# Optimization experiments

Hardware: AMD Instinct MI355X
Metric: run time of the kernel (lower is better)

Reference implementation:

```python
import jax, jax.numpy as jnp
import numpy as np

NV, NC, E, H, L = 100_000, 420_000, 630_000, 128, 8
ALPHA, THETA = 0.1, 0.5


def _seg_mean(msgs, dst, n_dst):
    # mean aggregation over destination segments (PyG SAGEConv default)
    s = jax.ops.segment_sum(msgs, dst, num_segments=n_dst)
    cnt = jax.ops.segment_sum(jnp.ones((dst.shape[0], 1), msgs.dtype), dst, num_segments=n_dst)
    return s / jnp.maximum(cnt, 1.0)


def _sage(x_src, x_dst, src, dst, n_dst, Wl, bl, Wr):
    # SAGEConv: lin_l(mean_{j in N(i)} x_j) + lin_r(x_i); lin_r has no bias
    agg = _seg_mean(x_src[src], dst, n_dst)
    return agg @ Wl + bl + x_dst @ Wr


def setup_inputs() -> dict:
    key = jax.random.key(0)
    ks = jax.random.split(key, 40)
    k = iter(range(40))
    rn = lambda shape, s=0.05: jax.random.normal(ks[next(k)], shape, jnp.float32) * s
    inp = {}
    inp['x_variable'] = jax.random.normal(ks[next(k)], (NV, 4), jnp.float32)
    inp['x_clause'] = jax.random.normal(ks[next(k)], (NC, 1), jnp.float32)
    src_p = jax.random.randint(ks[next(k)], (E,), 0, NV)
    dst_p = jax.random.randint(ks[next(k)], (E,), 0, NC)
    src_n = jax.random.randint(ks[next(k)], (E,), 0, NV)
    dst_n = jax.random.randint(ks[next(k)], (E,), 0, NC)
    inp['edge_pos'] = jnp.stack([src_p, dst_p])  # variable -> clause
    inp['edge_neg'] = jnp.stack([src_n, dst_n])
    inp['W_vemb'] = rn((4, H)); inp['b_vemb'] = rn((H,))
    inp['W_cemb'] = rn((1, H)); inp['b_cemb'] = rn((H,))
    for tag in ('pos', 'neg', 'rpos', 'rneg'):
        inp[f'Wl_{tag}'] = rn((L, H, H)); inp[f'bl_{tag}'] = rn((L, H))
        inp[f'Wr_{tag}'] = rn((L, H, H))
    inp['Wv'] = rn((L, H, H)); inp['bv'] = rn((L, H))
    inp['W_fin'] = rn((H, 1)); inp['b_fin'] = rn((1,))
    return inp


def reference(x_variable, x_clause, edge_pos, edge_neg,
              W_vemb, b_vemb, W_cemb, b_cemb,
              Wl_pos, bl_pos, Wr_pos, Wl_neg, bl_neg, Wr_neg,
              Wl_rpos, bl_rpos, Wr_rpos, Wl_rneg, bl_rneg, Wr_rneg,
              Wv, bv, W_fin, b_fin):
    v_h0 = jax.nn.relu(x_variable @ W_vemb + b_vemb)
    c_h0 = jax.nn.relu(x_clause @ W_cemb + b_cemb)
    v_h, c_h = v_h0, c_h0
    sp, dp = edge_pos[0], edge_pos[1]
    sn, dn = edge_neg[0], edge_neg[1]
    for i in range(L):
        v_old = v_h
        # HeteroConv(aggr='sum'): clause gets pos_in + neg_in, variable gets rev_pos_in + rev_neg_in
        c_new = (_sage(v_h, c_h, sp, dp, NC, Wl_pos[i], bl_pos[i], Wr_pos[i]) +
                 _sage(v_h, c_h, sn, dn, NC, Wl_neg[i], bl_neg[i], Wr_neg[i]))
        v_new = (_sage(c_h, v_h, dp, sp, NV, Wl_rpos[i], bl_rpos[i], Wr_rpos[i]) +
                 _sage(c_h, v_h, dn, sn, NV, Wl_rneg[i], bl_rneg[i], Wr_rneg[i]))
        v_h = (1.0 - ALPHA) * v_new + ALPHA * v_h0
        c_h = (1.0 - ALPHA) * c_new + ALPHA * c_h0
        beta = float(np.log(THETA / (i + 1) + 1.0))
        v_h = (1.0 - beta) * v_h + beta * (v_h @ Wv[i] + bv[i])
        v_h = v_h + v_old  # use_inter_layer_res=True
        v_h, c_h = jax.nn.relu(v_h), jax.nn.relu(c_h)
    return v_h @ W_fin + b_fin
```

## Files before the change

### kernel.cpp

```cpp
#include <hip/hip_runtime.h>
#include <math.h>

#define NVV 100000
#define NCC 420000
#define EE  630000
#define HH  128
#define LL  8

typedef unsigned int uint;
typedef unsigned short ushort;
typedef __attribute__((ext_vector_type(8))) short bf16x8;
typedef __attribute__((ext_vector_type(4))) float f32x4;

#define MFMA16(a,b,c) __builtin_amdgcn_mfma_f32_16x16x32_bf16(a,b,c,0,0,0)
#define SW(r,k) (((r)<<7) + ((k) ^ (((r)&7)<<3)))

__device__ inline float bf2f(uint u){ return __uint_as_float(u << 16); }
__device__ inline uint  f2bf(float f){
  uint b = __float_as_uint(f);
  return (b + 0x7FFFu + ((b >> 16) & 1u)) >> 16;
}
__device__ inline uint pack2(float a, float b){ return f2bf(a) | (f2bf(b) << 16); }
__device__ inline float4 relu4(float4 v){
  v.x = fmaxf(v.x, 0.f); v.y = fmaxf(v.y, 0.f);
  v.z = fmaxf(v.z, 0.f); v.w = fmaxf(v.w, 0.f);
  return v;
}

__global__ void k_sentinel(float* out, float v){
  if (blockIdx.x == 0 && threadIdx.x == 0) out[0] = v;
}

__device__ inline float4 vemb4(const float* __restrict__ xv, const float* __restrict__ W,
                               const float* __restrict__ b, int i, int h4){
  float x0 = xv[4*i+0], x1 = xv[4*i+1], x2 = xv[4*i+2], x3 = xv[4*i+3];
  float4 w0 = *(const float4*)(W + 0*HH + h4);
  float4 w1 = *(const float4*)(W + 1*HH + h4);
  float4 w2 = *(const float4*)(W + 2*HH + h4);
  float4 w3 = *(const float4*)(W + 3*HH + h4);
  float4 bb = *(const float4*)(b + h4);
  float4 r;
  r.x = fmaf(x0,w0.x, fmaf(x1,w1.x, fmaf(x2,w2.x, fmaf(x3,w3.x, bb.x))));
  r.y = fmaf(x0,w0.y, fmaf(x1,w1.y, fmaf(x2,w2.y, fmaf(x3,w3.y, bb.y))));
  r.z = fmaf(x0,w0.z, fmaf(x1,w1.z, fmaf(x2,w2.z, fmaf(x3,w3.z, bb.z))));
  r.w = fmaf(x0,w0.w, fmaf(x1,w1.w, fmaf(x2,w2.w, fmaf(x3,w3.w, bb.w))));
  return r;
}

__global__ void k_embed_v(const float* __restrict__ xv, const float* __restrict__ W,
                          const float* __restrict__ b, float* __restrict__ out){
  int tid = blockIdx.x * 256 + threadIdx.x;
  int i = tid >> 5;
  if (i >= NVV) return;
  int h4 = (tid & 31) << 2;
  *(float4*)(out + (size_t)i*HH + h4) = relu4(vemb4(xv, W, b, i, h4));
}

__global__ void k_embed_c(const float* __restrict__ xc, const float* __restrict__ W,
                          const float* __restrict__ b, uint* __restrict__ out){
  int tid = blockIdx.x * 256 + threadIdx.x;
  int i = tid >> 5;
  if (i >= NCC) return;
  int c2 = tid & 31;
  int h4 = c2 << 2;
  float x0 = xc[i];
  float4 w = *(const float4*)(W + h4);
  float4 bb = *(const float4*)(b + h4);
  float4 r;
  r.x = fmaxf(fmaf(x0, w.x, bb.x), 0.f);
  r.y = fmaxf(fmaf(x0, w.y, bb.y), 0.f);
  r.z = fmaxf(fmaf(x0, w.z, bb.z), 0.f);
  r.w = fmaxf(fmaf(x0, w.w, bb.w), 0.f);
  uint2 o; o.x = pack2(r.x, r.y); o.y = pack2(r.z, r.w);
  *(uint2*)(out + (size_t)i*64 + c2*2) = o;
}

__global__ void k_prep(const float* __restrict__ Wl_pos, const float* __restrict__ Wl_neg,
                       const float* __restrict__ Wl_rpos, const float* __restrict__ Wl_rneg,
                       const float* __restrict__ Wv, const float* __restrict__ Wr_pos,
                       const float* __restrict__ Wr_neg, const float* __restrict__ Wr_rpos,
                       const float* __restrict__ Wr_rneg, ushort* __restrict__ wt){
  int tid = blockIdx.x * 256 + threadIdx.x;
  int n4 = tid & 31, k = (tid >> 5) & 127, l = (tid >> 12) & 7, m = tid >> 15;
  const float* s1; const float* s2 = nullptr;
  switch (m){
    case 0: s1 = Wl_pos;  break;
    case 1: s1 = Wl_neg;  break;
    case 2: s1 = Wl_rpos; break;
    case 3: s1 = Wl_rneg; break;
    case 4: s1 = Wv;      break;
    case 5: s1 = Wr_pos;  s2 = Wr_neg;  break;
    default: s1 = Wr_rpos; s2 = Wr_rneg; break;
  }
  size_t o = (size_t)l*16384 + (size_t)k*128 + n4*4;
  float4 w = *(const float4*)(s1 + o);
  if (s2){
    float4 w2 = *(const float4*)(s2 + o);
    w.x += w2.x; w.y += w2.y; w.z += w2.z; w.w += w2.w;
  }
  ushort* hi = wt + (size_t)((m*LL + l)*2    )*16384;
  ushort* lo = wt + (size_t)((m*LL + l)*2 + 1)*16384;
  float vv[4] = {w.x, w.y, w.z, w.w};
  #pragma unroll
  for (int e = 0; e < 4; ++e){
    int n = n4*4 + e;
    uint h = f2bf(vv[e]);
    float r = vv[e] - bf2f(h);
    hi[SW(n, k)] = (ushort)h;
    lo[SW(n, k)] = (ushort)f2bf(r);
  }
}

__global__ void k_counti(const int* __restrict__ d, int* cnt, int n){
  int i = blockIdx.x * 256 + threadIdx.x;
  if (i < n) atomicAdd(&cnt[d[i]], 1);
}

#define SCAN256(ts, t) \
  for (int off = 1; off < 256; off <<= 1){ \
    int _a = (t >= off) ? ts[t - off] : 0; \
    __syncthreads(); \
    ts[t] += _a; \
    __syncthreads(); \
  }

__global__ void k_scanb(const int* __restrict__ in, int* __restrict__ out,
                        int* __restrict__ part, int n){
  __shared__ int ts[256];
  int b = blockIdx.x, t = threadIdx.x;
  int base = b*1024 + t*4;
  int v0 = (base+0 < n) ? in[base+0] : 0;
  int v1 = (base+1 < n) ? in[base+1] : 0;
  int v2 = (base+2 < n) ? in[base+2] : 0;
  int v3 = (base+3 < n) ? in[base+3] : 0;
  int s1 = v0, s2 = s1+v1, s3 = s2+v2, tsum = s3+v3;
  ts[t] = tsum; __syncthreads();
  SCAN256(ts, t)
  int excl = ts[t] - tsum;
  if (base+0 < n) out[base+0] = excl;
  if (base+1 < n) out[base+1] = excl + s1;
  if (base+2 < n) out[base+2] = excl + s2;
  if (base+3 < n) out[base+3] = excl + s3;
  if (t == 255) part[b] = ts[255];
}

__global__ void k_scanp(int* p, int nb){
  __shared__ int ts[256];
  __shared__ int carry;
  int t = threadIdx.x;
  if (t == 0) carry = 0;
  __syncthreads();
  for (int c = 0; c*256 < nb; ++c){
    int i = c*256 + t;
    int v = (i < nb) ? p[i] : 0;
    ts[t] = v; __syncthreads();
    SCAN256(ts, t)
    int excl = ts[t] - v + carry;
    if (i < nb) p[i] = excl;
    int tot = ts[255];
    __syncthreads();
    if (t == 0) carry += tot;
    __syncthreads();
  }
}

__global__ void k_scana(int* out, const int* __restrict__ part, int n){
  int i = blockIdx.x * 256 + threadIdx.x;
  if (i < n) out[i] += part[i >> 10];
}

__global__ void k_fill(const int* __restrict__ dst, const int* __restrict__ pay,
                       int* cur, int* __restrict__ eo, int n){
  int i = blockIdx.x * 256 + threadIdx.x;
  if (i >= n) return;
  int p = atomicAdd(&cur[dst[i]], 1);
  eo[p] = pay[i];
}

__global__ void k_vgather(const uint* __restrict__ ch,
                          const int* __restrict__ ipp, const int* __restrict__ epp,
                          const int* __restrict__ ipn, const int* __restrict__ epn,
                          uint* __restrict__ Up, uint* __restrict__ Un){
  int g = blockIdx.x * 256 + threadIdx.x;
  int v = g >> 6, lane = g & 63;
  if (v >= NVV) return;
  int s = v ? ipp[v-1] : 0, e = ipp[v];
  float a0 = 0.f, a1 = 0.f;
  for (int j = s; j < e; ++j){
    uint u = ch[(size_t)epp[j]*64 + lane];
    a0 += bf2f(u & 0xFFFFu); a1 += bf2f(u >> 16);
  }
  float inv = 1.f / fmaxf((float)(e - s), 1.f);
  Up[(size_t)v*64 + lane] = pack2(a0*inv, a1*inv);
  s = v ? ipn[v-1] : 0; e = ipn[v];
  a0 = 0.f; a1 = 0.f;
  for (int j = s; j < e; ++j){
    uint u = ch[(size_t)epn[j]*64 + lane];
    a0 += bf2f(u & 0xFFFFu); a1 += bf2f(u >> 16);
  }
  inv = 1.f / fmaxf((float)(e - s), 1.f);
  Un[(size_t)v*64 + lane] = pack2(a0*inv, a1*inv);
}

__device__ inline void stA_bf16(const uint4* __restrict__ A, ushort* As, int m0, int M, int t){
  #pragma unroll
  for (int j = 0; j < 4; ++j){
    int idx = j*512 + t, r = idx >> 4, c = idx & 15;
    uint4 v = make_uint4(0,0,0,0);
    if (m0 + r < M) v = A[(size_t)(m0 + r)*16 + c];
    *(uint4*)(As + SW(r, c*8)) = v;
  }
}

__device__ inline void stA_f32(const float* __restrict__ A, ushort* As, int m0, int M, int t){
  const float4* A4 = (const float4*)A;
  #pragma unroll
  for (int j = 0; j < 8; ++j){
    int idx = j*512 + t, r = idx >> 5, c = idx & 31;
    float4 v = make_float4(0.f,0.f,0.f,0.f);
    if (m0 + r < M) v = A4[(size_t)(m0 + r)*32 + c];
    uint2 u; u.x = pack2(v.x, v.y); u.y = pack2(v.z, v.w);
    *(uint2*)(As + SW(r, c*4)) = u;
  }
}

__device__ inline void stB(const uint4* __restrict__ Bt, ushort* Bs, int t){
  #pragma unroll
  for (int j = 0; j < 4; ++j) ((uint4*)Bs)[j*512 + t] = Bt[j*512 + t];
}

__device__ inline void kloop(const ushort* As, const ushort* Bs, int wr, int wc,
                             int l15, int g, f32x4 acc[2][4]){
  #pragma unroll
  for (int kk = 0; kk < 4; ++kk){
    int kb = kk*32 + g*8;
    bf16x8 a0 = *(const bf16x8*)(As + SW(wr*32 + l15,      kb));
    bf16x8 a1 = *(const bf16x8*)(As + SW(wr*32 + 16 + l15, kb));
    #pragma unroll
    for (int ni = 0; ni < 4; ++ni){
      int n = wc*64 + ni*16 + l15;
      bf16x8 b = *(const bf16x8*)(Bs + SW(n, kb));
      acc[0][ni] = MFMA16(a0, b, acc[0][ni]);
      acc[1][ni] = MFMA16(a1, b, acc[1][ni]);
    }
  }
}

__device__ inline void accStoreF(float* ldsF, f32x4 acc[2][4], int wr, int wc, int l15, int g){
  #pragma unroll
  for (int mi = 0; mi < 2; ++mi)
    #pragma unroll
    for (int ni = 0; ni < 4; ++ni)
      #pragma unroll
      for (int j = 0; j < 4; ++j)
        ldsF[(wr*32 + mi*16 + g*4 + j)*128 + wc*64 + ni*16 + l15] = acc[mi][ni][j];
}

__device__ inline void accStoreFsw(float* ldsF, f32x4 acc[2][4], int wr, int wc, int l15, int g){
  #pragma unroll
  for (int mi = 0; mi < 2; ++mi)
    #pragma unroll
    for (int ni = 0; ni < 4; ++ni)
      #pragma unroll
      for (int j = 0; j < 4; ++j){
        int r = wr*32 + mi*16 + g*4 + j;
        int c = wc*64 + ni*16 + l15;
        ldsF[r*128 + (((c >> 2) ^ (r & 31)) << 2) + (c & 3)] = acc[mi][ni][j];
      }
}

__device__ inline void accStoreBf(ushort* dst, f32x4 acc[2][4], int wr, int wc, int l15, int g){
  #pragma unroll
  for (int mi = 0; mi < 2; ++mi)
    #pragma unroll
    for (int ni = 0; ni < 4; ++ni)
      #pragma unroll
      for (int j = 0; j < 4; ++j)
        dst[(wr*32 + mi*16 + g*4 + j)*128 + wc*64 + ni*16 + l15] =
            (ushort)f2bf(acc[mi][ni][j]);
}

#define MMHEAD \
  __shared__ ushort lds[32768]; \
  ushort* As = lds; ushort* Bs = lds + 16384; \
  int t = threadIdx.x, m0 = blockIdx.x * 128; \
  int w = t >> 6, l = t & 63, wr = w >> 1, wc = w & 1, l15 = l & 15, g = l >> 4; \
  const f32x4 zz = {0.f, 0.f, 0.f, 0.f};

__global__ __launch_bounds__(512) void k_mm_dual(const float* __restrict__ A,
    const uint4* __restrict__ Bph, const uint4* __restrict__ Bpl,
    const uint4* __restrict__ Bnh, const uint4* __restrict__ Bnl,
    uint4* __restrict__ Up, uint4* __restrict__ Un, int M){
  MMHEAD
  f32x4 accP[2][4], accN[2][4];
  #pragma unroll
  for (int mi = 0; mi < 2; ++mi)
    #pragma unroll
    for (int ni = 0; ni < 4; ++ni){ accP[mi][ni] = zz; accN[mi][ni] = zz; }
  stA_f32(A, As, m0, M, t);
  stB(Bph, Bs, t); __syncthreads();
  kloop(As, Bs, wr, wc, l15, g, accP); __syncthreads();
  stB(Bpl, Bs, t); __syncthreads();
  kloop(As, Bs, wr, wc, l15, g, accP); __syncthreads();
  stB(Bnh, Bs, t); __syncthreads();
  kloop(As, Bs, wr, wc, l15, g, accN); __syncthreads();
  stB(Bnl, Bs, t); __syncthreads();
  kloop(As, Bs, wr, wc, l15, g, accN); __syncthreads();
  accStoreBf(lds,         accP, wr, wc, l15, g);
  accStoreBf(lds + 16384, accN, wr, wc, l15, g);
  __syncthreads();
  #pragma unroll
  for (int j = 0; j < 4; ++j){
    int idx = j*512 + t, r = idx >> 4, c = idx & 15;
    if (m0 + r < M){
      Up[(size_t)(m0 + r)*16 + c] = ((const uint4*)lds)[idx];
      Un[(size_t)(m0 + r)*16 + c] = ((const uint4*)(lds + 16384))[idx];
    }
  }
}

__global__ __launch_bounds__(512) void k_mm3(const uint4* __restrict__ Ap,
    const uint4* __restrict__ An, const float* __restrict__ Af,
    const uint4* __restrict__ Bph, const uint4* __restrict__ Bpl,
    const uint4* __restrict__ Bnh, const uint4* __restrict__ Bnl,
    const uint4* __restrict__ Bfh, const uint4* __restrict__ Bfl,
    const float* __restrict__ xv, const float* __restrict__ Wve, const float* __restrict__ bve,
    const float* __restrict__ blp, const float* __restrict__ bln,
    uint2* __restrict__ vmid, int M){
  MMHEAD
  f32x4 acc[2][4];
  #pragma unroll
  for (int mi = 0; mi < 2; ++mi)
    #pragma unroll
    for (int ni = 0; ni < 4; ++ni) acc[mi][ni] = zz;

  stA_bf16(Ap, As, m0, M, t); stB(Bph, Bs, t); __syncthreads();
  kloop(As, Bs, wr, wc, l15, g, acc); __syncthreads();
  stB(Bpl, Bs, t); __syncthreads();
  kloop(As, Bs, wr, wc, l15, g, acc); __syncthreads();

  stA_bf16(An, As, m0, M, t); stB(Bnh, Bs, t); __syncthreads();
  kloop(As, Bs, wr, wc, l15, g, acc); __syncthreads();
  stB(Bnl, Bs, t); __syncthreads();
  kloop(As, Bs, wr, wc, l15, g, acc); __syncthreads();

  stA_f32(Af, As, m0, M, t); stB(Bfh, Bs, t); __syncthreads();
  kloop(As, Bs, wr, wc, l15, g, acc); __syncthreads();
  stB(Bfl, Bs, t); __syncthreads();
  kloop(As, Bs, wr, wc, l15, g, acc); __syncthreads();

  float* ldsF = (float*)lds;
  accStoreF(ldsF, acc, wr, wc, l15, g);
  __syncthreads();
  #pragma unroll
  for (int j = 0; j < 8; ++j){
    int idx = j*512 + t, r = idx >> 5, c4 = idx & 31;
    int row = m0 + r;
    if (row >= M) continue;
    float4 a4 = ((const float4*)ldsF)[r*32 + c4];
    float4 bp = ((const float4*)blp)[c4];
    float4 bn = ((const float4*)bln)[c4];
    float4 w0 = ((const float4*)Wve)[0*32 + c4];
    float4 w1 = ((const float4*)Wve)[1*32 + c4];
    float4 w2 = ((const float4*)Wve)[2*32 + c4];
    float4 w3 = ((const float4*)Wve)[3*32 + c4];
    float4 bb = ((const float4*)bve)[c4];
    float4 xx = *(const float4*)(xv + (size_t)row*4);
    float4 h;
    h.x = fmaf(xx.x,w0.x, fmaf(xx.y,w1.x, fmaf(xx.z,w2.x, fmaf(xx.w,w3.x, bb.x))));
    h.y = fmaf(xx.x,w0.y, fmaf(xx.y,w1.y, fmaf(xx.z,w2.y, fmaf(xx.w,w3.y, bb.y))));
    h.z = fmaf(xx.x,w0.z, fmaf(xx.y,w1.z, fmaf(xx.z,w2.z, fmaf(xx.w,w3.z, bb.z))));
    h.w = fmaf(xx.x,w0.w, fmaf(xx.y,w1.w, fmaf(xx.z,w2.w, fmaf(xx.w,w3.w, bb.w))));
    h = relu4(h);
    float4 o;
    o.x = 0.9f*(a4.x + bp.x + bn.x) + 0.1f*h.x;
    o.y = 0.9f*(a4.y + bp.y + bn.y) + 0.1f*h.y;
    o.z = 0.9f*(a4.z + bp.z + bn.z) + 0.1f*h.z;
    o.w = 0.9f*(a4.w + bp.w + bn.w) + 0.1f*h.w;
    uint2 u; u.x = pack2(o.x, o.y); u.y = pack2(o.z, o.w);
    vmid[(size_t)row*32 + c4] = u;
  }
}

__global__ __launch_bounds__(512) void k_mm_f(const uint4* __restrict__ Avm,
    const uint4* __restrict__ Bh, const uint4* __restrict__ Bl,
    const uint2* __restrict__ vmid, const float* __restrict__ bvv,
    float omb, float beta, float* vh, int M){
  MMHEAD
  f32x4 acc[2][4];
  #pragma unroll
  for (int mi = 0; mi < 2; ++mi)
    #pragma unroll
    for (int ni = 0; ni < 4; ++ni) acc[mi][ni] = zz;
  stA_bf16(Avm, As, m0, M, t); stB(Bh, Bs, t); __syncthreads();
  kloop(As, Bs, wr, wc, l15, g, acc); __syncthreads();
  stB(Bl, Bs, t); __syncthreads();
  kloop(As, Bs, wr, wc, l15, g, acc); __syncthreads();
  float* ldsF = (float*)lds;
  accStoreF(ldsF, acc, wr, wc, l15, g);
  __syncthreads();
  #pragma unroll
  for (int j = 0; j < 8; ++j){
    int idx = j*512 + t, r = idx >> 5, c4 = idx & 31;
    int row = m0 + r;
    if (row >= M) continue;
    float4 a4 = ((const float4*)ldsF)[r*32 + c4];
    uint2 um = vmid[(size_t)row*32 + c4];
    float4 bb = ((const float4*)bvv)[c4];
    float4 vo = *(const float4*)(vh + (size_t)row*HH + c4*4);
    float m0f = bf2f(um.x & 0xFFFFu), m1f = bf2f(um.x >> 16);
    float m2f = bf2f(um.y & 0xFFFFu), m3f = bf2f(um.y >> 16);
    float4 o;
    o.x = fmaxf(omb*m0f + beta*(a4.x + bb.x) + vo.x, 0.f);
    o.y = fmaxf(omb*m1f + beta*(a4.y + bb.y) + vo.y, 0.f);
    o.z = fmaxf(omb*m2f + beta*(a4.z + bb.z) + vo.z, 0.f);
    o.w = fmaxf(omb*m3f + beta*(a4.w + bb.w) + vo.w, 0.f);
    *(float4*)(vh + (size_t)row*HH + c4*4) = o;
  }
}

__global__ __launch_bounds__(512) void k_mm_c(const uint4* ch,
    const uint4* __restrict__ Bh, const uint4* __restrict__ Bl,
    const int* __restrict__ ipp, const int* __restrict__ epp,
    const int* __restrict__ ipn, const int* __restrict__ epn,
    const uint4* __restrict__ Yp, const uint4* __restrict__ Yn,
    const float* __restrict__ xc, const float* __restrict__ Wc, const float* __restrict__ bc,
    const float* __restrict__ blp, const float* __restrict__ bln,
    uint2* chout){
  MMHEAD
  f32x4 acc[2][4];
  #pragma unroll
  for (int mi = 0; mi < 2; ++mi)
    #pragma unroll
    for (int ni = 0; ni < 4; ++ni) acc[mi][ni] = zz;
  stA_bf16(ch, As, m0, NCC, t); stB(Bh, Bs, t); __syncthreads();
  kloop(As, Bs, wr, wc, l15, g, acc); __syncthreads();
  stB(Bl, Bs, t); __syncthreads();
  kloop(As, Bs, wr, wc, l15, g, acc); __syncthreads();
  float* ldsF = (float*)lds;
  accStoreFsw(ldsF, acc, wr, wc, l15, g);
  __syncthreads();

  int r = t >> 2, q = t & 3, row = m0 + r;
  if (row >= NCC) return;
  float4 ga[8];
  #pragma unroll
  for (int m = 0; m < 8; ++m) ga[m] = make_float4(0.f,0.f,0.f,0.f);
  int s = row ? ipp[row-1] : 0, e = ipp[row];
  for (int j = s; j < e; ++j){
    const uint4* yr = Yp + (size_t)epp[j]*16 + q*4;
    #pragma unroll
    for (int m = 0; m < 4; ++m){
      uint4 u = yr[m];
      ga[2*m].x   += bf2f(u.x & 0xFFFFu); ga[2*m].y   += bf2f(u.x >> 16);
      ga[2*m].z   += bf2f(u.y & 0xFFFFu); ga[2*m].w   += bf2f(u.y >> 16);
      ga[2*m+1].x += bf2f(u.z & 0xFFFFu); ga[2*m+1].y += bf2f(u.z >> 16);
      ga[2*m+1].z += bf2f(u.w & 0xFFFFu); ga[2*m+1].w += bf2f(u.w >> 16);
    }
  }
  float invp = 1.f / fmaxf((float)(e - s), 1.f);
  #pragma unroll
  for (int m = 0; m < 8; ++m){
    ga[m].x *= invp; ga[m].y *= invp; ga[m].z *= invp; ga[m].w *= invp;
  }
  s = row ? ipn[row-1] : 0; e = ipn[row];
  float invn = 1.f / fmaxf((float)(e - s), 1.f);
  for (int j = s; j < e; ++j){
    const uint4* yr = Yn + (size_t)epn[j]*16 + q*4;
    #pragma unroll
    for (int m = 0; m < 4; ++m){
      uint4 u = yr[m];
      ga[2*m].x   = fmaf(bf2f(u.x & 0xFFFFu), invn, ga[2*m].x);
      ga[2*m].y   = fmaf(bf2f(u.x >> 16),     invn, ga[2*m].y);
      ga[2*m].z   = fmaf(bf2f(u.y & 0xFFFFu), invn, ga[2*m].z);
      ga[2*m].w   = fmaf(bf2f(u.y >> 16),     invn, ga[2*m].w);
      ga[2*m+1].x = fmaf(bf2f(u.z & 0xFFFFu), invn, ga[2*m+1].x);
      ga[2*m+1].y = fmaf(bf2f(u.z >> 16),     invn, ga[2*m+1].y);
      ga[2*m+1].z = fmaf(bf2f(u.w & 0xFFFFu), invn, ga[2*m+1].z);
      ga[2*m+1].w = fmaf(bf2f(u.w >> 16),     invn, ga[2*m+1].w);
    }
  }
  float xcv = xc[row];
  #pragma unroll
  for (int m = 0; m < 8; ++m){
    int gi = q*8 + m;
    float4 res = ((const float4*)ldsF)[r*32 + (gi ^ (r & 31))];
    float4 wc  = ((const float4*)Wc)[gi];
    float4 bcv = ((const float4*)bc)[gi];
    float4 bp  = ((const float4*)blp)[gi];
    float4 bn  = ((const float4*)bln)[gi];
    float4 h;
    h.x = fmaxf(fmaf(xcv, wc.x, bcv.x), 0.f);
    h.y = fmaxf(fmaf(xcv, wc.y, bcv.y), 0.f);
    h.z = fmaxf(fmaf(xcv, wc.z, bcv.z), 0.f);
    h.w = fmaxf(fmaf(xcv, wc.w, bcv.w), 0.f);
    float4 o;
    o.x = fmaxf(0.9f*(ga[m].x + res.x + bp.x + bn.x) + 0.1f*h.x, 0.f);
    o.y = fmaxf(0.9f*(ga[m].y + res.y + bp.y + bn.y) + 0.1f*h.y, 0.f);
    o.z = fmaxf(0.9f*(ga[m].z + res.z + bp.z + bn.z) + 0.1f*h.z, 0.f);
    o.w = fmaxf(0.9f*(ga[m].w + res.w + bp.w + bn.w) + 0.1f*h.w, 0.f);
    uint2 u2; u2.x = pack2(o.x, o.y); u2.y = pack2(o.z, o.w);
    chout[(size_t)row*32 + gi] = u2;
  }
}

__global__ void k_final(const float* __restrict__ vh, const float* __restrict__ wf,
                        const float* __restrict__ bf, float* __restrict__ out){
  int wid = (blockIdx.x * 256 + threadIdx.x) >> 6;
  if (wid >= NVV) return;
  int lane = threadIdx.x & 63;
  float2 a = *(const float2*)(vh + (size_t)wid*HH + lane*2);
  float2 w = *(const float2*)(wf + lane*2);
  float s = a.x*w.x + a.y*w.y;
  #pragma unroll
  for (int off = 32; off > 0; off >>= 1) s += __shfl_down(s, off);
  if (lane == 0) out[wid] = s + bf[0];
}

extern "C" void kernel_launch(void* const* d_in, const int* in_sizes, int n_in,
                              void* d_out, int out_size, void* d_ws, size_t ws_size,
                              hipStream_t stream) {
  const float* xv  = (const float*)d_in[0];
  const float* xc  = (const float*)d_in[1];
  const int*   ep  = (const int*)d_in[2];
  const int*   en  = (const int*)d_in[3];
  const float* Wve = (const float*)d_in[4];
  const float* bve = (const float*)d_in[5];
  const float* Wce = (const float*)d_in[6];
  const float* bce = (const float*)d_in[7];
  const float* Wl_pos  = (const float*)d_in[8];
  const float* bl_pos  = (const float*)d_in[9];
  const float* Wr_pos  = (const float*)d_in[10];
  const float* Wl_neg  = (const float*)d_in[11];
  const float* bl_neg  = (const float*)d_in[12];
  const float* Wr_neg  = (const float*)d_in[13];
  const float* Wl_rpos = (const float*)d_in[14];
  const float* bl_rpos = (const float*)d_in[15];
  const float* Wr_rpos = (const float*)d_in[16];
  const float* Wl_rneg = (const float*)d_in[17];
  const float* bl_rneg = (const float*)d_in[18];
  const float* Wr_rneg = (const float*)d_in[19];
  const float* Wv  = (const float*)d_in[20];
  const float* bv  = (const float*)d_in[21];
  const float* Wf  = (const float*)d_in[22];
  const float* bf  = (const float*)d_in[23];
  float* out = (float*)d_out;

  size_t off = 0;
  auto alloc = [&](size_t bytes) -> void* {
    void* p = (char*)d_ws + off;
    off = (off + bytes + 255) & ~(size_t)255;
    return p;
  };
  uint*   c_h  = (uint*)  alloc((size_t)NCC*64*sizeof(uint));
  float*  v_h  = (float*) alloc((size_t)NVV*HH*sizeof(float));
  uint*   U1   = (uint*)  alloc((size_t)NVV*64*sizeof(uint));
  uint*   U2   = (uint*)  alloc((size_t)NVV*64*sizeof(uint));
  uint*   vmid = (uint*)  alloc((size_t)NVV*64*sizeof(uint));
  ushort* wt   = (ushort*)alloc((size_t)7*LL*2*16384*sizeof(ushort));
  int* ipc_p = (int*)alloc((size_t)NCC*sizeof(int));
  int* ec_p  = (int*)alloc((size_t)EE*sizeof(int));
  int* ipc_n = (int*)alloc((size_t)NCC*sizeof(int));
  int* ec_n  = (int*)alloc((size_t)EE*sizeof(int));
  int* ipv_p = (int*)alloc((size_t)NVV*sizeof(int));
  int* ev_p  = (int*)alloc((size_t)EE*sizeof(int));
  int* ipv_n = (int*)alloc((size_t)NVV*sizeof(int));
  int* ev_n  = (int*)alloc((size_t)EE*sizeof(int));
  int* cnt   = (int*)alloc((size_t)NCC*sizeof(int));
  int* part  = (int*)alloc(4096);
  if (off > ws_size){
    k_sentinel<<<1, 64, 0, stream>>>(out, (float)(ws_size >> 20));
    return;
  }

  const int TB = 256;
  const int gE  = (EE + TB-1)/TB;
  const int gV  = (NVV*32 + TB-1)/TB;
  const int gC  = (NCC*32 + TB-1)/TB;
  const int gGv = (NVV + 127)/128;
  const int gGc = (NCC + 127)/128;
  const int gWd = (NVV*64 + TB-1)/TB;

  auto wp = [&](int m, int l, int h) -> const uint4* {
    return (const uint4*)(wt + (size_t)((m*LL + l)*2 + h)*16384);
  };

  auto build = [&](const int* dst, const int* pay, int nd, int* ip, int* eo){
    hipMemsetAsync(cnt, 0, (size_t)nd*sizeof(int), stream);
    k_counti<<<gE, TB, 0, stream>>>(dst, cnt, EE);
    int nb = (nd + 1023)/1024;
    k_scanb<<<nb, TB, 0, stream>>>(cnt, ip, part, nd);
    k_scanp<<<1, TB, 0, stream>>>(part, nb);
    k_scana<<<(nd + TB-1)/TB, TB, 0, stream>>>(ip, part, nd);
    k_fill<<<gE, TB, 0, stream>>>(dst, pay, ip, eo, EE);
  };
  build(ep + EE, ep,      NCC, ipc_p, ec_p);
  build(en + EE, en,      NCC, ipc_n, ec_n);
  build(ep,      ep + EE, NVV, ipv_p, ev_p);
  build(en,      en + EE, NVV, ipv_n, ev_n);

  k_prep<<<(7*LL*128*32)/TB, TB, 0, stream>>>(Wl_pos, Wl_neg, Wl_rpos, Wl_rneg, Wv,
                                              Wr_pos, Wr_neg, Wr_rpos, Wr_rneg, wt);

  k_embed_v<<<gV, TB, 0, stream>>>(xv, Wve, bve, v_h);
  k_embed_c<<<gC, TB, 0, stream>>>(xc, Wce, bce, c_h);

  for (int l = 0; l < LL; ++l){
    const size_t bo = (size_t)l*HH;
    double beta_d = log(0.5/(double)(l+1) + 1.0);

    k_vgather<<<gWd, TB, 0, stream>>>(c_h, ipv_p, ev_p, ipv_n, ev_n, U1, U2);
    k_mm3<<<gGv, 512, 0, stream>>>((const uint4*)U1, (const uint4*)U2, v_h,
                                   wp(2,l,0), wp(2,l,1), wp(3,l,0), wp(3,l,1),
                                   wp(6,l,0), wp(6,l,1),
                                   xv, Wve, bve, bl_rpos + bo, bl_rneg + bo,
                                   (uint2*)vmid, NVV);
    k_mm_dual<<<gGv, 512, 0, stream>>>(v_h, wp(0,l,0), wp(0,l,1), wp(1,l,0), wp(1,l,1),
                                       (uint4*)U1, (uint4*)U2, NVV);
    k_mm_c<<<gGc, 512, 0, stream>>>((const uint4*)c_h, wp(5,l,0), wp(5,l,1),
                                    ipc_p, ec_p, ipc_n, ec_n,
                                    (const uint4*)U1, (const uint4*)U2,
                                    xc, Wce, bce, bl_pos + bo, bl_neg + bo,
                                    (uint2*)c_h);
    k_mm_f<<<gGv, 512, 0, stream>>>((const uint4*)vmid, wp(4,l,0), wp(4,l,1),
                                    (const uint2*)vmid, bv + bo,
                                    (float)(1.0 - beta_d), (float)beta_d, v_h, NVV);
  }

  k_final<<<gWd, TB, 0, stream>>>(v_h, Wf, bf, out);
}
```

Measured before the change: 3.774 ms.

## Fuse variable-side matmuls into one kernel and interleave pos/neg gathers

Merges the three variable-side kernels (aggregate+root matmul, Y projections, residual Wv matmul) into one kernel. It reuses the v_h tile already in LDS for the Y projections and keeps vmid in LDS instead of round-tripping it through global memory. It also interleaves the positive and negative neighbor loops in both gather kernels to expose more memory-level parallelism, and reuses the CSR index buffer as the count buffer. The trade-offs are more register pressure and a longer serial chain per block. Another risk: the fused kernel writes Y into U1/U2 while other blocks may still be reading those buffers as aggregation inputs, but each block reads and writes only its own rows, so this is safe.

```diff
diff --git a/kernel.cpp b/kernel.cpp
--- a/kernel.cpp
+++ b/kernel.cpp
@@ -184,22 +184,29 @@
   int g = blockIdx.x * 256 + threadIdx.x;
   int v = g >> 6, lane = g & 63;
   if (v >= NVV) return;
-  int s = v ? ipp[v-1] : 0, e = ipp[v];
-  float a0 = 0.f, a1 = 0.f;
-  for (int j = s; j < e; ++j){
-    uint u = ch[(size_t)epp[j]*64 + lane];
-    a0 += bf2f(u & 0xFFFFu); a1 += bf2f(u >> 16);
-  }
-  float inv = 1.f / fmaxf((float)(e - s), 1.f);
-  Up[(size_t)v*64 + lane] = pack2(a0*inv, a1*inv);
-  s = v ? ipn[v-1] : 0; e = ipn[v];
-  a0 = 0.f; a1 = 0.f;
-  for (int j = s; j < e; ++j){
-    uint u = ch[(size_t)epn[j]*64 + lane];
-    a0 += bf2f(u & 0xFFFFu); a1 += bf2f(u >> 16);
-  }
-  inv = 1.f / fmaxf((float)(e - s), 1.f);
-  Un[(size_t)v*64 + lane] = pack2(a0*inv, a1*inv);
+  int sp = v ? ipp[v-1] : 0, ePos = ipp[v];
+  int sn = v ? ipn[v-1] : 0, eNeg = ipn[v];
+  float p0 = 0.f, p1 = 0.f, n0 = 0.f, n1 = 0.f;
+  int jp = sp, jn = sn;
+  while (jp < ePos && jn < eNeg){
+    uint up = ch[(size_t)epp[jp]*64 + lane];
+    uint un = ch[(size_t)epn[jn]*64 + lane];
+    p0 += bf2f(up & 0xFFFFu); p1 += bf2f(up >> 16);
+    n0 += bf2f(un & 0xFFFFu); n1 += bf2f(un >> 16);
+    ++jp; ++jn;
+  }
+  for (; jp < ePos; ++jp){
+    uint up = ch[(size_t)epp[jp]*64 + lane];
+    p0 += bf2f(up & 0xFFFFu); p1 += bf2f(up >> 16);
+  }
+  for (; jn < eNeg; ++jn){
+    uint un = ch[(size_t)epn[jn]*64 + lane];
+    n0 += bf2f(un & 0xFFFFu); n1 += bf2f(un >> 16);
+  }
+  float ivp = 1.f / fmaxf((float)(ePos - sp), 1.f);
+  float ivn = 1.f / fmaxf((float)(eNeg - sn), 1.f);
+  Up[(size_t)v*64 + lane] = pack2(p0*ivp, p1*ivp);
+  Un[(size_t)v*64 + lane] = pack2(n0*ivn, n1*ivn);
 }
 
 __device__ inline void stA_bf16(const uint4* __restrict__ A, ushort* As, int m0, int M, int t){
@@ -283,29 +290,53 @@
 #define MMHEAD \
   __shared__ ushort lds[32768]; \
   ushort* As = lds; ushort* Bs = lds + 16384; \
+  float* accumF = (float*)lds; \
   int t = threadIdx.x, m0 = blockIdx.x * 128; \
   int w = t >> 6, l = t & 63, wr = w >> 1, wc = w & 1, l15 = l & 15, g = l >> 4; \
-  const f32x4 zz = {0.f, 0.f, 0.f, 0.f};
-
-__global__ __launch_bounds__(512) void k_mm_dual(const float* __restrict__ A,
+  const f32x4 zz = {0.f, 0.f, 0.f, 0.f}; \
+  (void)accumF;
+
+#define ZACC(A) { \
+  _Pragma("unroll") for (int mi_ = 0; mi_ < 2; ++mi_) \
+    _Pragma("unroll") for (int ni_ = 0; ni_ < 4; ++ni_) A[mi_][ni_] = zz; }
+
+__global__ __launch_bounds__(512) void k_fused_v(
+    const uint4* __restrict__ AggP, const uint4* __restrict__ AggN,
     const uint4* __restrict__ Bph, const uint4* __restrict__ Bpl,
     const uint4* __restrict__ Bnh, const uint4* __restrict__ Bnl,
-    uint4* __restrict__ Up, uint4* __restrict__ Un, int M){
+    const uint4* __restrict__ Bfh, const uint4* __restrict__ Bfl,
+    const uint4* __restrict__ Byph, const uint4* __restrict__ Bypl,
+    const uint4* __restrict__ Bynh, const uint4* __restrict__ Bynl,
+    const uint4* __restrict__ Bvh, const uint4* __restrict__ Bvl,
+    const float* __restrict__ xv, const float* __restrict__ Wve, const float* __restrict__ bve,
+    const float* __restrict__ blp, const float* __restrict__ bln, const float* __restrict__ bvv,
+    float omb, float beta,
+    uint4* __restrict__ Yp, uint4* __restrict__ Yn, float* vh, int M){
   MMHEAD
-  f32x4 accP[2][4], accN[2][4];
-  #pragma unroll
-  for (int mi = 0; mi < 2; ++mi)
-    #pragma unroll
-    for (int ni = 0; ni < 4; ++ni){ accP[mi][ni] = zz; accN[mi][ni] = zz; }
-  stA_f32(A, As, m0, M, t);
-  stB(Bph, Bs, t); __syncthreads();
+  f32x4 accM[2][4], accP[2][4], accN[2][4];
+  ZACC(accM) ZACC(accP) ZACC(accN)
+
+  stA_bf16(AggP, As, m0, M, t); stB(Bph, Bs, t); __syncthreads();
+  kloop(As, Bs, wr, wc, l15, g, accM); __syncthreads();
+  stB(Bpl, Bs, t); __syncthreads();
+  kloop(As, Bs, wr, wc, l15, g, accM); __syncthreads();
+  stA_bf16(AggN, As, m0, M, t); stB(Bnh, Bs, t); __syncthreads();
+  kloop(As, Bs, wr, wc, l15, g, accM); __syncthreads();
+  stB(Bnl, Bs, t); __syncthreads();
+  kloop(As, Bs, wr, wc, l15, g, accM); __syncthreads();
+  stA_f32(vh, As, m0, M, t); stB(Bfh, Bs, t); __syncthreads();
+  kloop(As, Bs, wr, wc, l15, g, accM); __syncthreads();
+  stB(Bfl, Bs, t); __syncthreads();
+  kloop(As, Bs, wr, wc, l15, g, accM); __syncthreads();
+  stB(Byph, Bs, t); __syncthreads();
   kloop(As, Bs, wr, wc, l15, g, accP); __syncthreads();
-  stB(Bpl, Bs, t); __syncthreads();
+  stB(Bypl, Bs, t); __syncthreads();
   kloop(As, Bs, wr, wc, l15, g, accP); __syncthreads();
-  stB(Bnh, Bs, t); __syncthreads();
+  stB(Bynh, Bs, t); __syncthreads();
   kloop(As, Bs, wr, wc, l15, g, accN); __syncthreads();
-  stB(Bnl, Bs, t); __syncthreads();
+  stB(Bynl, Bs, t); __syncthreads();
   kloop(As, Bs, wr, wc, l15, g, accN); __syncthreads();
+
   accStoreBf(lds,         accP, wr, wc, l15, g);
   accStoreBf(lds + 16384, accN, wr, wc, l15, g);
   __syncthreads();
@@ -313,132 +344,96 @@
   for (int j = 0; j < 4; ++j){
     int idx = j*512 + t, r = idx >> 4, c = idx & 15;
     if (m0 + r < M){
-      Up[(size_t)(m0 + r)*16 + c] = ((const uint4*)lds)[idx];
-      Un[(size_t)(m0 + r)*16 + c] = ((const uint4*)(lds + 16384))[idx];
+      Yp[(size_t)(m0 + r)*16 + c] = ((const uint4*)lds)[idx];
+      Yn[(size_t)(m0 + r)*16 + c] = ((const uint4*)(lds + 16384))[idx];
     }
   }
-}
-
-__global__ __launch_bounds__(512) void k_mm3(const uint4* __restrict__ Ap,
-    const uint4* __restrict__ An, const float* __restrict__ Af,
-    const uint4* __restrict__ Bph, const uint4* __restrict__ Bpl,
-    const uint4* __restrict__ Bnh, const uint4* __restrict__ Bnl,
-    const uint4* __restrict__ Bfh, const uint4* __restrict__ Bfl,
-    const float* __restrict__ xv, const float* __restrict__ Wve, const float* __restrict__ bve,
-    const float* __restrict__ blp, const float* __restrict__ bln,
-    uint2* __restrict__ vmid, int M){
-  MMHEAD
-  f32x4 acc[2][4];
-  #pragma unroll
-  for (int mi = 0; mi < 2; ++mi)
-    #pragma unroll
-    for (int ni = 0; ni < 4; ++ni) acc[mi][ni] = zz;
-
-  stA_bf16(Ap, As, m0, M, t); stB(Bph, Bs, t); __syncthreads();
-  kloop(As, Bs, wr, wc, l15, g, acc); __syncthreads();
-  stB(Bpl, Bs, t); __syncthreads();
-  kloop(As, Bs, wr, wc, l15, g, acc); __syncthreads();
-
-  stA_bf16(An, As, m0, M, t); stB(Bnh, Bs, t); __syncthreads();
-  kloop(As, Bs, wr, wc, l15, g, acc); __syncthreads();
-  stB(Bnl, Bs, t); __syncthreads();
-  kloop(As, Bs, wr, wc, l15, g, acc); __syncthreads();
-
-  stA_f32(Af, As, m0, M, t); stB(Bfh, Bs, t); __syncthreads();
-  kloop(As, Bs, wr, wc, l15, g, acc); __syncthreads();
-  stB(Bfl, Bs, t); __syncthreads();
-  kloop(As, Bs, wr, wc, l15, g, acc); __syncthreads();
-
-  float* ldsF = (float*)lds;
-  accStoreF(ldsF, acc, wr, wc, l15, g);
   __syncthreads();
+
+  accStoreF(accumF, accM, wr, wc, l15, g);
+  __syncthreads();
+  float4 vreg[8];
   #pragma unroll
   for (int j = 0; j < 8; ++j){
     int idx = j*512 + t, r = idx >> 5, c4 = idx & 31;
     int row = m0 + r;
-    if (row >= M) continue;
-    float4 a4 = ((const float4*)ldsF)[r*32 + c4];
-    float4 bp = ((const float4*)blp)[c4];
-    float4 bn = ((const float4*)bln)[c4];
-    float4 w0 = ((const float4*)Wve)[0*32 + c4];
-    float4 w1 = ((const float4*)Wve)[1*32 + c4];
-    float4 w2 = ((const float4*)Wve)[2*32 + c4];
-    float4 w3 = ((const float4*)Wve)[3*32 + c4];
-    float4 bb = ((const float4*)bve)[c4];
-    float4 xx = *(const float4*)(xv + (size_t)row*4);
-    float4 h;
-    h.x = fmaf(xx.x,w0.x, fmaf(xx.y,w1.x, fmaf(xx.z,w2.x, fmaf(xx.w,w3.x, bb.x))));
-    h.y = fmaf(xx.x,w0.y, fmaf(xx.y,w1.y, fmaf(xx.z,w2.y, fmaf(xx.w,w3.y, bb.y))));
-    h.z = fmaf(xx.x,w0.z, fmaf(xx.y,w1.z, fmaf(xx.z,w2.z, fmaf(xx.w,w3.z, bb.z))));
-    h.w = fmaf(xx.x,w0.w, fmaf(xx.y,w1.w, fmaf(xx.z,w2.w, fmaf(xx.w,w3.w, bb.w))));
-    h = relu4(h);
-    float4 o;
-    o.x = 0.9f*(a4.x + bp.x + bn.x) + 0.1f*h.x;
-    o.y = 0.9f*(a4.y + bp.y + bn.y) + 0.1f*h.y;
-    o.z = 0.9f*(a4.z + bp.z + bn.z) + 0.1f*h.z;
-    o.w = 0.9f*(a4.w + bp.w + bn.w) + 0.1f*h.w;
-    uint2 u; u.x = pack2(o.x, o.y); u.y = pack2(o.z, o.w);
-    vmid[(size_t)row*32 + c4] = u;
-  }
-}
-
-__global__ __launch_bounds__(512) void k_mm_f(const uint4* __restrict__ Avm,
-    const uint4* __restrict__ Bh, const uint4* __restrict__ Bl,
-    const uint2* __restrict__ vmid, const float* __restrict__ bvv,
-    float omb, float beta, float* vh, int M){
-  MMHEAD
-  f32x4 acc[2][4];
+    float4 o = make_float4(0.f,0.f,0.f,0.f);
+    if (row < M){
+      float4 a4 = ((const float4*)accumF)[r*32 + c4];
+      float4 bp = ((const float4*)blp)[c4];
+      float4 bn = ((const float4*)bln)[c4];
+      float4 h = relu4(vemb4(xv, Wve, bve, row, c4*4));
+      o.x = 0.9f*(a4.x + bp.x + bn.x) + 0.1f*h.x;
+      o.y = 0.9f*(a4.y + bp.y + bn.y) + 0.1f*h.y;
+      o.z = 0.9f*(a4.z + bp.z + bn.z) + 0.1f*h.z;
+      o.w = 0.9f*(a4.w + bp.w + bn.w) + 0.1f*h.w;
+    }
+    vreg[j] = o;
+  }
+  __syncthreads();
+  #pragma unroll
+  for (int j = 0; j < 8; ++j){
+    int idx = j*512 + t, r = idx >> 5, c4 = idx & 31;
+    uint2 u; u.x = pack2(vreg[j].x, vreg[j].y); u.y = pack2(vreg[j].z, vreg[j].w);
+    *(uint2*)(As + SW(r, c4*4)) = u;
+  }
+  f32x4 accT[2][4];
+  ZACC(accT)
+  stB(Bvh, Bs, t); __syncthreads();
+  kloop(As, Bs, wr, wc, l15, g, accT); __syncthreads();
+  stB(Bvl, Bs, t); __syncthreads();
+  kloop(As, Bs, wr, wc, l15, g, accT);
+
   #pragma unroll
   for (int mi = 0; mi < 2; ++mi)
     #pragma unroll
-    for (int ni = 0; ni < 4; ++ni) acc[mi][ni] = zz;
-  stA_bf16(Avm, As, m0, M, t); stB(Bh, Bs, t); __syncthreads();
-  kloop(As, Bs, wr, wc, l15, g, acc); __syncthreads();
-  stB(Bl, Bs, t); __syncthreads();
-  kloop(As, Bs, wr, wc, l15, g, acc); __syncthreads();
-  float* ldsF = (float*)lds;
-  accStoreF(ldsF, acc, wr, wc, l15, g);
-  __syncthreads();
-  #pragma unroll
-  for (int j = 0; j < 8; ++j){
-    int idx = j*512 + t, r = idx >> 5, c4 = idx & 31;
-    int row = m0 + r;
-    if (row >= M) continue;
-    float4 a4 = ((const float4*)ldsF)[r*32 + c4];
-    uint2 um = vmid[(size_t)row*32 + c4];
-    float4 bb = ((const float4*)bvv)[c4];
-    float4 vo = *(const float4*)(vh + (size_t)row*HH + c4*4);
-    float m0f = bf2f(um.x & 0xFFFFu), m1f = bf2f(um.x >> 16);
-    float m2f = bf2f(um.y & 0xFFFFu), m3f = bf2f(um.y >> 16);
-    float4 o;
-    o.x = fmaxf(omb*m0f + beta*(a4.x + bb.x) + vo.x, 0.f);
-    o.y = fmaxf(omb*m1f + beta*(a4.y + bb.y) + vo.y, 0.f);
-    o.z = fmaxf(omb*m2f + beta*(a4.z + bb.z) + vo.z, 0.f);
-    o.w = fmaxf(omb*m3f + beta*(a4.w + bb.w) + vo.w, 0.f);
-    *(float4*)(vh + (size_t)row*HH + c4*4) = o;
+    for (int ni = 0; ni < 4; ++ni)
+      #pragma unroll
+      for (int j = 0; j < 4; ++j){
+        int lr  = wr*32 + mi*16 + g*4 + j;
+        int col = wc*64 + ni*16 + l15;
+        int grow = m0 + lr;
+        if (grow < M){
+          float vm = bf2f((uint)As[SW(lr, col)]);
+          float vo = vh[(size_t)grow*HH + col];
+          float o  = fmaxf(omb*vm + beta*(accT[mi][ni][j] + bvv[col]) + vo, 0.f);
+          vh[(size_t)grow*HH + col] = o;
+        }
+      }
+}
+
+__device__ inline void acc_yrow(float4 ga[8], uint4 u0, uint4 u1, uint4 u2, uint4 u3, float sc){
+  uint4 uu[4] = {u0, u1, u2, u3};
+  #pragma unroll
+  for (int m = 0; m < 4; ++m){
+    uint4 u = uu[m];
+    ga[2*m].x   = fmaf(bf2f(u.x & 0xFFFFu), sc, ga[2*m].x);
+    ga[2*m].y   = fmaf(bf2f(u.x >> 16),     sc, ga[2*m].y);
+    ga[2*m].z   = fmaf(bf2f(u.y & 0xFFFFu), sc, ga[2*m].z);
+    ga[2*m].w   = fmaf(bf2f(u.y >> 16),     sc, ga[2*m].w);
+    ga[2*m+1].x = fmaf(bf2f(u.z & 0xFFFFu), sc, ga[2*m+1].x);
+    ga[2*m+1].y = fmaf(bf2f(u.z >> 16),     sc, ga[2*m+1].y);
+    ga[2*m+1].z = fmaf(bf2f(u.w & 0xFFFFu), sc, ga[2*m+1].z);
+    ga[2*m+1].w = fmaf(bf2f(u.w >> 16),     sc, ga[2*m+1].w);
   }
 }
 
 __global__ __launch_bounds__(512) void k_mm_c(const uint4* ch,
     const uint4* __restrict__ Bh, const uint4* __restrict__ Bl,
-    const int* __restrict__ ipp, const int* __restrict__ epp,
-    const int* __restrict__ ipn, const int* __restrict__ epn,
+    const int* __restrict__ ipp, const int* __restrict__ ecp,
+    const int* __restrict__ ipn, const int* __restrict__ ecn,
     const uint4* __restrict__ Yp, const uint4* __restrict__ Yn,
     const float* __restrict__ xc, const float* __restrict__ Wc, const float* __restrict__ bc,
     const float* __restrict__ blp, const float* __restrict__ bln,
     uint2* chout){
   MMHEAD
   f32x4 acc[2][4];
-  #pragma unroll
-  for (int mi = 0; mi < 2; ++mi)
-    #pragma unroll
-    for (int ni = 0; ni < 4; ++ni) acc[mi][ni] = zz;
+  ZACC(acc)
   stA_bf16(ch, As, m0, NCC, t); stB(Bh, Bs, t); __syncthreads();
   kloop(As, Bs, wr, wc, l15, g, acc); __syncthreads();
   stB(Bl, Bs, t); __syncthreads();
   kloop(As, Bs, wr, wc, l15, g, acc); __syncthreads();
-  float* ldsF = (float*)lds;
-  accStoreFsw(ldsF, acc, wr, wc, l15, g);
+  accStoreFsw(accumF, acc, wr, wc, l15, g);
   __syncthreads();
 
   int r = t >> 2, q = t & 3, row = m0 + r;
@@ -446,54 +441,44 @@
   float4 ga[8];
   #pragma unroll
   for (int m = 0; m < 8; ++m) ga[m] = make_float4(0.f,0.f,0.f,0.f);
-  int s = row ? ipp[row-1] : 0, e = ipp[row];
-  for (int j = s; j < e; ++j){
-    const uint4* yr = Yp + (size_t)epp[j]*16 + q*4;
-    #pragma unroll
-    for (int m = 0; m < 4; ++m){
-      uint4 u = yr[m];
-      ga[2*m].x   += bf2f(u.x & 0xFFFFu); ga[2*m].y   += bf2f(u.x >> 16);
-      ga[2*m].z   += bf2f(u.y & 0xFFFFu); ga[2*m].w   += bf2f(u.y >> 16);
-      ga[2*m+1].x += bf2f(u.z & 0xFFFFu); ga[2*m+1].y += bf2f(u.z >> 16);
-      ga[2*m+1].z += bf2f(u.w & 0xFFFFu); ga[2*m+1].w += bf2f(u.w >> 16);
-    }
-  }
-  float invp = 1.f / fmaxf((float)(e - s), 1.f);
-  #pragma unroll
-  for (int m = 0; m < 8; ++m){
-    ga[m].x *= invp; ga[m].y *= invp; ga[m].z *= invp; ga[m].w *= invp;
-  }
-  s = row ? ipn[row-1] : 0; e = ipn[row];
-  float invn = 1.f / fmaxf((float)(e - s), 1.f);
-  for (int j = s; j < e; ++j){
-    const uint4* yr = Yn + (size_t)epn[j]*16 + q*4;
-    #pragma unroll
-    for (int m = 0; m < 4; ++m){
-      uint4 u = yr[m];
-      ga[2*m].x   = fmaf(bf2f(u.x & 0xFFFFu), invn, ga[2*m].x);
-      ga[2*m].y   = fmaf(bf2f(u.x >> 16),     invn, ga[2*m].y);
-      ga[2*m].z   = fmaf(bf2f(u.y & 0xFFFFu), invn, ga[2*m].z);
-      ga[2*m].w   = fmaf(bf2f(u.y >> 16),     invn, ga[2*m].w);
-      ga[2*m+1].x = fmaf(bf2f(u.z & 0xFFFFu), invn, ga[2*m+1].x);
-      ga[2*m+1].y = fmaf(bf2f(u.z >> 16),     invn, ga[2*m+1].y);
-      ga[2*m+1].z = fmaf(bf2f(u.w & 0xFFFFu), invn, ga[2*m+1].z);
-      ga[2*m+1].w = fmaf(bf2f(u.w >> 16),     invn, ga[2*m+1].w);
-    }
+  int sp = row ? ipp[row-1] : 0, ePos = ipp[row];
+  int sn = row ? ipn[row-1] : 0, eNeg = ipn[row];
+  float invp = 1.f / fmaxf((float)(ePos - sp), 1.f);
+  float invn = 1.f / fmaxf((float)(eNeg - sn), 1.f);
+  int jp = sp, jn = sn;
+  while (jp < ePos && jn < eNeg){
+    const uint4* yp = Yp + (size_t)ecp[jp]*16 + q*4;
+    const uint4* yn = Yn + (size_t)ecn[jn]*16 + q*4;
+    uint4 a0 = yp[0], a1 = yp[1], a2 = yp[2], a3 = yp[3];
+    uint4 b0 = yn[0], b1 = yn[1], b2 = yn[2], b3 = yn[3];
+    acc_yrow(ga, a0, a1, a2, a3, invp);
+    acc_yrow(ga, b0, b1, b2, b3, invn);
+    ++jp; ++jn;
+  }
+  while (jp < ePos){
+    const uint4* yp = Yp + (size_t)ecp[jp]*16 + q*4;
+    acc_yrow(ga, yp[0], yp[1], yp[2], yp[3], invp);
+    ++jp;
+  }
+  while (jn < eNeg){
+    const uint4* yn = Yn + (size_t)ecn[jn]*16 + q*4;
+    acc_yrow(ga, yn[0], yn[1], yn[2], yn[3], invn);
+    ++jn;
   }
   float xcv = xc[row];
   #pragma unroll
   for (int m = 0; m < 8; ++m){
     int gi = q*8 + m;
-    float4 res = ((const float4*)ldsF)[r*32 + (gi ^ (r & 31))];
-    float4 wc  = ((const float4*)Wc)[gi];
+    float4 res = ((const float4*)accumF)[r*32 + (gi ^ (r & 31))];
+    float4 wc4 = ((const float4*)Wc)[gi];
     float4 bcv = ((const float4*)bc)[gi];
     float4 bp  = ((const float4*)blp)[gi];
     float4 bn  = ((const float4*)bln)[gi];
     float4 h;
-    h.x = fmaxf(fmaf(xcv, wc.x, bcv.x), 0.f);
-    h.y = fmaxf(fmaf(xcv, wc.y, bcv.y), 0.f);
-    h.z = fmaxf(fmaf(xcv, wc.z, bcv.z), 0.f);
-    h.w = fmaxf(fmaf(xcv, wc.w, bcv.w), 0.f);
+    h.x = fmaxf(fmaf(xcv, wc4.x, bcv.x), 0.f);
+    h.y = fmaxf(fmaf(xcv, wc4.y, bcv.y), 0.f);
+    h.z = fmaxf(fmaf(xcv, wc4.z, bcv.z), 0.f);
+    h.w = fmaxf(fmaf(xcv, wc4.w, bcv.w), 0.f);
     float4 o;
     o.x = fmaxf(0.9f*(ga[m].x + res.x + bp.x + bn.x) + 0.1f*h.x, 0.f);
     o.y = fmaxf(0.9f*(ga[m].y + res.y + bp.y + bn.y) + 0.1f*h.y, 0.f);
@@ -556,18 +541,16 @@
   float*  v_h  = (float*) alloc((size_t)NVV*HH*sizeof(float));
   uint*   U1   = (uint*)  alloc((size_t)NVV*64*sizeof(uint));
   uint*   U2   = (uint*)  alloc((size_t)NVV*64*sizeof(uint));
-  uint*   vmid = (uint*)  alloc((size_t)NVV*64*sizeof(uint));
   ushort* wt   = (ushort*)alloc((size_t)7*LL*2*16384*sizeof(ushort));
-  int* ipc_p = (int*)alloc((size_t)NCC*sizeof(int));
-  int* ec_p  = (int*)alloc((size_t)EE*sizeof(int));
-  int* ipc_n = (int*)alloc((size_t)NCC*sizeof(int));
-  int* ec_n  = (int*)alloc((size_t)EE*sizeof(int));
-  int* ipv_p = (int*)alloc((size_t)NVV*sizeof(int));
-  int* ev_p  = (int*)alloc((size_t)EE*sizeof(int));
-  int* ipv_n = (int*)alloc((size_t)NVV*sizeof(int));
-  int* ev_n  = (int*)alloc((size_t)EE*sizeof(int));
-  int* cnt   = (int*)alloc((size_t)NCC*sizeof(int));
-  int* part  = (int*)alloc(4096);
+  int*   ipc_p = (int*)  alloc((size_t)NCC*sizeof(int));
+  int*   ec_p  = (int*)  alloc((size_t)EE*sizeof(int));
+  int*   ipc_n = (int*)  alloc((size_t)NCC*sizeof(int));
+  int*   ec_n  = (int*)  alloc((size_t)EE*sizeof(int));
+  int*   ipv_p = (int*)  alloc((size_t)NVV*sizeof(int));
+  int*   ev_p  = (int*)  alloc((size_t)EE*sizeof(int));
+  int*   ipv_n = (int*)  alloc((size_t)NVV*sizeof(int));
+  int*   ev_n  = (int*)  alloc((size_t)EE*sizeof(int));
+  int*   part  = (int*)  alloc(4096);
   if (off > ws_size){
     k_sentinel<<<1, 64, 0, stream>>>(out, (float)(ws_size >> 20));
     return;
@@ -586,10 +569,10 @@
   };
 
   auto build = [&](const int* dst, const int* pay, int nd, int* ip, int* eo){
-    hipMemsetAsync(cnt, 0, (size_t)nd*sizeof(int), stream);
-    k_counti<<<gE, TB, 0, stream>>>(dst, cnt, EE);
+    hipMemsetAsync(ip, 0, (size_t)nd*sizeof(int), stream);
+    k_counti<<<gE, TB, 0, stream>>>(dst, ip, EE);
     int nb = (nd + 1023)/1024;
-    k_scanb<<<nb, TB, 0, stream>>>(cnt, ip, part, nd);
+    k_scanb<<<nb, TB, 0, stream>>>(ip, ip, part, nd);
     k_scanp<<<1, TB, 0, stream>>>(part, nb);
     k_scana<<<(nd + TB-1)/TB, TB, 0, stream>>>(ip, part, nd);
     k_fill<<<gE, TB, 0, stream>>>(dst, pay, ip, eo, EE);
@@ -610,21 +593,19 @@
     double beta_d = log(0.5/(double)(l+1) + 1.0);
 
     k_vgather<<<gWd, TB, 0, stream>>>(c_h, ipv_p, ev_p, ipv_n, ev_n, U1, U2);
-    k_mm3<<<gGv, 512, 0, stream>>>((const uint4*)U1, (const uint4*)U2, v_h,
-                                   wp(2,l,0), wp(2,l,1), wp(3,l,0), wp(3,l,1),
-                                   wp(6,l,0), wp(6,l,1),
-                                   xv, Wve, bve, bl_rpos + bo, bl_rneg + bo,
-                                   (uint2*)vmid, NVV);
-    k_mm_dual<<<gGv, 512, 0, stream>>>(v_h, wp(0,l,0), wp(0,l,1), wp(1,l,0), wp(1,l,1),
-                                       (uint4*)U1, (uint4*)U2, NVV);
+    k_fused_v<<<gGv, 512, 0, stream>>>((const uint4*)U1, (const uint4*)U2,
+                                       wp(2,l,0), wp(2,l,1), wp(3,l,0), wp(3,l,1),
+                                       wp(6,l,0), wp(6,l,1),
+                                       wp(0,l,0), wp(0,l,1), wp(1,l,0), wp(1,l,1),
+                                       wp(4,l,0), wp(4,l,1),
+                                       xv, Wve, bve, bl_rpos + bo, bl_rneg + bo, bv + bo,
+                                       (float)(1.0 - beta_d), (float)beta_d,
+                                       (uint4*)U1, (uint4*)U2, v_h, NVV);
     k_mm_c<<<gGc, 512, 0, stream>>>((const uint4*)c_h, wp(5,l,0), wp(5,l,1),
                                     ipc_p, ec_p, ipc_n, ec_n,
                                     (const uint4*)U1, (const uint4*)U2,
                                     xc, Wce, bce, bl_pos + bo, bl_neg + bo,
                                     (uint2*)c_h);
-    k_mm_f<<<gGv, 512, 0, stream>>>((const uint4*)vmid, wp(4,l,0), wp(4,l,1),
-                                    (const uint2*)vmid, bv + bo,
-                                    (float)(1.0 - beta_d), (float)beta_d, v_h, NVV);
   }
 
   k_final<<<gWd, TB, 0, stream>>>(v_h, Wf, bf, out);
```

New measurement: 3.794 ms. Within noise of the previous version (+0.5%).
